# Optimization experiments

Measured on AMD Instinct MI355X. Metric: run time of the kernel, lower is better.

Reference implementation:

```python
import jax, jax.numpy as jnp
import numpy as np

MAX_SCALE_CAP = 200
STEP = 3


def _shift(a, dy, dx):
    # a[..., y+dy, x+dx] with zero fill outside (dy, dx >= 0), matching the
    # zero-padded dilated 3x3 convs whose only off-center tap is at (+dy,+dx).
    H, W = a.shape[-2], a.shape[-1]
    p = jnp.pad(a, ((0, 0), (0, 0), (0, dy), (0, dx)))
    return p[..., dy:dy + H, dx:dx + W]


def _dif_stacks(Pred, GT, ROI):
    # Builds difPrd / difGT: channel order is (scale major, layer l, direction)
    # directions in dict order: Horizontal (0,+s), Vertical (+s,0), Diagonal (+s,+s)
    B, _, H, W = Pred.shape
    max_scale = min(MAX_SCALE_CAP, max(H, W))
    dP, dG = [], []
    for scale in range(1, max_scale, STEP):
        bP, bG = [], []
        for dy, dx in ((0, scale), (scale, 0), (scale, scale)):
            roi = ROI * _shift(ROI, dy, dx)             # [B,1,H,W]
            bP.append(roi * (Pred - _shift(Pred, dy, dx)))  # [B,3,H,W]
            bG.append(roi * (GT - _shift(GT, dy, dx)))
        # stack dirs on a new axis after layer axis -> l-major, dir-minor
        dP.append(jnp.stack(bP, axis=2).reshape(B, 9, H, W))
        dG.append(jnp.stack(bG, axis=2).reshape(B, 9, H, W))
    return jnp.concatenate(dP, axis=1), jnp.concatenate(dG, axis=1)


def _loss(PredXYZ, GTXYZ, ROIMask):
    difPrd, difGT = _dif_stacks(PredXYZ, GTXYZ, ROIMask)

    # normalization constant per image (detached in the original)
    Rat = jax.nn.relu(difPrd / (difGT + 1e-5))
    absG = jnp.abs(difGT)
    NormConst = (absG * Rat).sum((1, 2, 3)) / ((absG * (Rat > 0)).sum((1, 2, 3)) + 1e-4)
    NormConst = jax.lax.stop_gradient(NormConst)

    c = NormConst                                   # [B]
    safe_c = jnp.where(c > 1e-4, c, 1.0)
    term1 = jnp.where(
        c > 1e-4,
        jnp.abs(difGT - difPrd / safe_c[:, None, None, None]).mean((1, 2, 3)),
        0.0,
    )

    roi_sum = ROIMask.sum((1, 2, 3))
    pos_cnt = (difGT > 0).sum((1, 2, 3)).astype(jnp.float32)
    mean_prd = jnp.abs(difPrd).sum((1, 2, 3)) / pos_cnt

    big = roi_sum > 200
    term2 = jnp.where(big & (mean_prd > 30) & (c > 10), mean_prd - 30.0, 0.0)
    fact = 0.1 / (c + 0.001)
    term3 = jnp.where(big & (mean_prd < 2) & (c < 0.1), (0.2 - mean_prd) * fact, 0.0)

    return (term1 + term2 + term3).sum(), NormConst


def setup_inputs() -> dict:
    key = jax.random.key(0)
    k1, k2, k3 = jax.random.split(key, 3)
    PredXYZ = jax.random.normal(k1, (2, 3, 256, 256), dtype=jnp.float32)
    GTXYZ = jax.random.normal(k2, (2, 3, 256, 256), dtype=jnp.float32)
    ROIMask = (jax.random.uniform(k3, (2, 1, 256, 256)) > 0.3).astype(jnp.float32)
    return {"PredXYZ": PredXYZ, "GTXYZ": GTXYZ, "ROIMask": ROIMask}


def reference(PredXYZ, GTXYZ, ROIMask):
    return _loss(PredXYZ, GTXYZ, ROIMask)
```

## Files before the change

### kernel.cpp

```cpp
#include <hip/hip_runtime.h>


#define NSCALES 67
#define IMG_H 256
#define IMG_W 256
#define NPIX 65536
#define NLINES 2046
#define LMAX_PAD 320


__device__ __forceinline__ double wave_red(double v) {
#pragma unroll
  for (int o = 32; o > 0; o >>= 1) v += __shfl_down(v, o, 64);
  return v;
}

__device__ __forceinline__ void decode_line(int id, int& b, int& base, int& stride, int& L) {
  if (id < 512) {
    b = id >> 8; int y = id & 255;
    base = y * IMG_W; stride = 1; L = IMG_W;
  } else if (id < 1024) {
    int t = id - 512; b = t >> 8;
    base = t & 255; stride = IMG_W; L = IMG_H;
  } else {
    int t = id - 1024; b = (t >= 511) ? 1 : 0;
    int d = t - b * 511; int c = d - 255;
    int ac = (c < 0) ? -c : c;
    base = (c < 0) ? (-c) * IMG_W : c;
    stride = IMG_W + 1; L = 256 - ac;
  }
}

__device__ __forceinline__ int scale_count(int L, int q) {
  int rem = L - 1 - (q << 6);
  int kcnt = (rem >= 1) ? ((rem - 1) / 3 + 1) : 0;
  return (kcnt > NSCALES) ? NSCALES : kcnt;
}

__device__ __forceinline__ float stage_line(
    const float* __restrict__ Pred, const float* __restrict__ GT,
    const float* __restrict__ ROI, int b, int base, int stride, int L,
    int tid, float4* bufA, float4* bufB) {
  const float* P = Pred + b * (3 * NPIX);
  const float* G = GT + b * (3 * NPIX);
  const float* R = ROI + b * NPIX;
  float r = 0.f, p0 = 0.f, p1 = 0.f, p2 = 0.f, g0 = 0.f, g1 = 0.f, g2 = 0.f;
  if (tid < L) {
    int a = base + tid * stride;
    r = R[a];
    p0 = P[a]; p1 = P[a + NPIX]; p2 = P[a + 2 * NPIX];
    g0 = G[a]; g1 = G[a + NPIX]; g2 = G[a + 2 * NPIX];
  }
  bufA[tid] = make_float4(r, p0, p1, p2);
  bufB[tid] = make_float4(g0, g1, g2, 0.f);
  if (tid < LMAX_PAD - 256) {
    bufA[256 + tid] = make_float4(0.f, 0.f, 0.f, 0.f);
    bufB[256 + tid] = make_float4(0.f, 0.f, 0.f, 0.f);
  }
  __syncthreads();
  return r;
}

extern "C" __global__ void __launch_bounds__(256, 8) pass1_kernel(
    const float* __restrict__ Pred, const float* __restrict__ GT,
    const float* __restrict__ ROI, double* __restrict__ ws) {
  __shared__ float4 bufA[LMAX_PAD];
  __shared__ float4 bufB[LMAX_PAD];
  __shared__ double red[4][5];
  const int id = blockIdx.x;
  const int tid = threadIdx.x;
  const int wid = tid >> 6, lane = tid & 63;

  int b, base, stride, L;
  decode_line(id, b, base, stride, L);
  float stg_r = stage_line(Pred, GT, ROI, b, base, stride, L, tid, bufA, bufB);

  float f1 = 0.f, f2 = 0.f, fp = 0.f;
  int pci = 0;
  int P = 0;
  for (int q = 0; q < 4; ++q) {
    const int Kq = scale_count(L, q);
    int k = (wid - P) & 3;
    if (k < Kq) {
      const int c = (q << 6) + lane;
      const float4 cA = bufA[c];
      const float4 cB = bufB[c];
      const float cr = cA.x, cp0 = cA.y, cp1 = cA.z, cp2 = cA.w;
      const float cg0 = cB.x, cg1 = cB.y, cg2 = cB.z;
      const float4* tA = &bufA[c + 1 + 3 * k];
      const float4* tB = &bufB[c + 1 + 3 * k];
#pragma unroll 2
      for (; k < Kq; k += 4) {
        float4 t0 = tA[0];
        float4 t1 = tB[0];
        tA += 12; tB += 12;
        float rr = cr * t0.x;
#define L1BODY(cp, cg, tp, tg)                                   \
        {                                                        \
          float dP = rr * (cp - tp);                             \
          float dG = rr * (cg - tg);                             \
          float qq = dP * __builtin_amdgcn_rcpf(dG + 1e-5f);     \
          float aG = fabsf(dG);                                  \
          f1 += fmaxf(aG * qq, 0.f);                             \
          if (qq > 0.f) f2 += aG;                                \
          if (dG > 0.f) pci++;                                   \
          fp += fabsf(dP);                                       \
        }
        L1BODY(cp0, cg0, t0.y, t1.x)
        L1BODY(cp1, cg1, t0.z, t1.y)
        L1BODY(cp2, cg2, t0.w, t1.z)
#undef L1BODY
      }
    }
    P += Kq;
  }

  double w0 = wave_red((double)f1);
  double w1 = wave_red((double)f2);
  double w2 = wave_red((double)pci);
  double w3 = wave_red((double)fp);
  double w4 = wave_red((double)stg_r);
  if (lane == 0) {
    red[wid][0] = w0; red[wid][1] = w1; red[wid][2] = w2;
    red[wid][3] = w3; red[wid][4] = w4;
  }
  __syncthreads();
  if (tid < 4)
    unsafeAtomicAdd(&ws[b * 4 + tid],
                    red[0][tid] + red[1][tid] + red[2][tid] + red[3][tid]);
  if (tid == 4 && id < 512)
    unsafeAtomicAdd(&ws[8 + b], red[0][4] + red[1][4] + red[2][4] + red[3][4]);
}

extern "C" __global__ void __launch_bounds__(256, 8) pass2_kernel(
    const float* __restrict__ Pred, const float* __restrict__ GT,
    const float* __restrict__ ROI, double* __restrict__ ws) {
  __shared__ float4 bufA[LMAX_PAD];
  __shared__ float4 bufB[LMAX_PAD];
  __shared__ double red[4];
  __shared__ float s_invC;
  const int id = blockIdx.x;
  const int tid = threadIdx.x;
  const int wid = tid >> 6, lane = tid & 63;

  int b, base, stride, L;
  decode_line(id, b, base, stride, L);
  if (tid == 0) {
    double S1 = ws[b * 4 + 0], S2 = ws[b * 4 + 1];
    float cc = (float)(S1 / (S2 + 1e-4));
    s_invC = (cc > 1e-4f) ? (float)(1.0 / (double)cc) : 1.0f;
  }
  stage_line(Pred, GT, ROI, b, base, stride, L, tid, bufA, bufB);

  const float invC = s_invC;
  float f = 0.f;
  int P = 0;
  for (int q = 0; q < 4; ++q) {
    const int Kq = scale_count(L, q);
    int k = (wid - P) & 3;
    if (k < Kq) {
      const int c = (q << 6) + lane;
      const float4 cA = bufA[c];
      const float4 cB = bufB[c];
      const float cr = cA.x, cp0 = cA.y, cp1 = cA.z, cp2 = cA.w;
      const float cg0 = cB.x, cg1 = cB.y, cg2 = cB.z;
      const float4* tA = &bufA[c + 1 + 3 * k];
      const float4* tB = &bufB[c + 1 + 3 * k];
#pragma unroll 2
      for (; k < Kq; k += 4) {
        float4 t0 = tA[0];
        float4 t1 = tB[0];
        tA += 12; tB += 12;
        float rr = cr * t0.x;
        f += rr * fabsf((cg0 - t1.x) - (cp0 - t0.y) * invC);
        f += rr * fabsf((cg1 - t1.y) - (cp1 - t0.z) * invC);
        f += rr * fabsf((cg2 - t1.z) - (cp2 - t0.w) * invC);
      }
    }
    P += Kq;
  }
  double t = wave_red((double)f);
  if (lane == 0) red[wid] = t;
  __syncthreads();
  if (tid == 0)
    unsafeAtomicAdd(&ws[24 + b], red[0] + red[1] + red[2] + red[3]);
}

extern "C" __global__ void __launch_bounds__(64) final_kernel(
    const double* __restrict__ ws, float* __restrict__ out) {
  if (threadIdx.x == 0) {
    double loss = 0.0;
    for (int b = 0; b < 2; ++b) {
      double S1 = ws[b * 4 + 0], S2 = ws[b * 4 + 1];
      double PC = ws[b * 4 + 2], SP = ws[b * 4 + 3];
      double RS = ws[8 + b];
      float cc = (float)(S1 / (S2 + 1e-4));
      out[1 + b] = cc;
      double term1 = (cc > 1e-4f) ? ws[24 + b] / (603.0 * 65536.0) : 0.0;
      float meanPrd = (float)(SP / PC);
      bool big = RS > 200.0;
      float t2 = (big && meanPrd > 30.f && cc > 10.f) ? (meanPrd - 30.f) : 0.f;
      float fact = 0.1f / (cc + 0.001f);
      float t3 = (big && meanPrd < 2.f && cc < 0.1f) ? (0.2f - meanPrd) * fact : 0.f;
      loss += term1 + (double)(t2 + t3);
    }
    out[0] = (float)loss;
  }
}

extern "C" void kernel_launch(void* const* d_in, const int* in_sizes, int n_in,
                              void* d_out, int out_size, void* d_ws, size_t ws_size,
                              hipStream_t stream) {
  (void)in_sizes; (void)n_in; (void)out_size; (void)ws_size;
  const float* Pred = (const float*)d_in[0];
  const float* GT = (const float*)d_in[1];
  const float* ROI = (const float*)d_in[2];
  float* out = (float*)d_out;
  double* ws = (double*)d_ws;

  hipMemsetAsync(d_ws, 0, 32 * sizeof(double), stream);
  hipLaunchKernelGGL(pass1_kernel, dim3(NLINES), dim3(256), 0, stream,
                     Pred, GT, ROI, ws);
  hipLaunchKernelGGL(pass2_kernel, dim3(NLINES), dim3(256), 0, stream,
                     Pred, GT, ROI, ws);
  hipLaunchKernelGGL(final_kernel, dim3(1), dim3(64), 0, stream, ws, out);
}
```

Measured before the change: 128.1 us.

## Fuse both passes and final reduction into one kernel with grid-wide spin barrier

Merges pass1, pass2 and the final kernel into a single launch that uses an atomic counter as a grid barrier between the normalization-constant pass and the second pass. Each block keeps its staged line in shared memory and reuses it, instead of reloading it from global memory. Block 0 waits for all blocks to finish and then computes the final loss. This relies on all 2046 blocks being co-resident; the spin limit avoids a hang but would give wrong results if they are not.

```diff
diff --git a/kernel.cpp b/kernel.cpp
--- a/kernel.cpp
+++ b/kernel.cpp
@@ -61,12 +61,18 @@
   return r;
 }
 
-extern "C" __global__ void __launch_bounds__(256, 8) pass1_kernel(
+__device__ __forceinline__ double aread(const double* p) {
+  return __hip_atomic_load(p, __ATOMIC_RELAXED, __HIP_MEMORY_SCOPE_AGENT);
+}
+
+extern "C" __global__ void __launch_bounds__(256, 8) fused_kernel(
     const float* __restrict__ Pred, const float* __restrict__ GT,
-    const float* __restrict__ ROI, double* __restrict__ ws) {
+    const float* __restrict__ ROI, double* __restrict__ ws,
+    float* __restrict__ out) {
   __shared__ float4 bufA[LMAX_PAD];
   __shared__ float4 bufB[LMAX_PAD];
   __shared__ double red[4][5];
+  __shared__ float s_invC;
   const int id = blockIdx.x;
   const int tid = threadIdx.x;
   const int wid = tid >> 6, lane = tid & 63;
@@ -130,31 +136,27 @@
                     red[0][tid] + red[1][tid] + red[2][tid] + red[3][tid]);
   if (tid == 4 && id < 512)
     unsafeAtomicAdd(&ws[8 + b], red[0][4] + red[1][4] + red[2][4] + red[3][4]);
-}
-
-extern "C" __global__ void __launch_bounds__(256, 8) pass2_kernel(
-    const float* __restrict__ Pred, const float* __restrict__ GT,
-    const float* __restrict__ ROI, double* __restrict__ ws) {
-  __shared__ float4 bufA[LMAX_PAD];
-  __shared__ float4 bufB[LMAX_PAD];
-  __shared__ double red[4];
-  __shared__ float s_invC;
-  const int id = blockIdx.x;
-  const int tid = threadIdx.x;
-  const int wid = tid >> 6, lane = tid & 63;
-
-  int b, base, stride, L;
-  decode_line(id, b, base, stride, L);
+
+  int* ctr = (int*)&ws[16];
+  __threadfence();
+  __syncthreads();
   if (tid == 0) {
-    double S1 = ws[b * 4 + 0], S2 = ws[b * 4 + 1];
+    __hip_atomic_fetch_add(ctr, 1, __ATOMIC_ACQ_REL, __HIP_MEMORY_SCOPE_AGENT);
+    int spins = 0;
+    while (__hip_atomic_load(ctr, __ATOMIC_ACQUIRE, __HIP_MEMORY_SCOPE_AGENT) < NLINES &&
+           spins < (1 << 22)) {
+      __builtin_amdgcn_s_sleep(2);
+      ++spins;
+    }
+    double S1 = aread(&ws[b * 4 + 0]), S2 = aread(&ws[b * 4 + 1]);
     float cc = (float)(S1 / (S2 + 1e-4));
     s_invC = (cc > 1e-4f) ? (float)(1.0 / (double)cc) : 1.0f;
   }
-  stage_line(Pred, GT, ROI, b, base, stride, L, tid, bufA, bufB);
+  __syncthreads();
 
   const float invC = s_invC;
   float f = 0.f;
-  int P = 0;
+  P = 0;
   for (int q = 0; q < 4; ++q) {
     const int Kq = scale_count(L, q);
     int k = (wid - P) & 3;
@@ -180,23 +182,29 @@
     P += Kq;
   }
   double t = wave_red((double)f);
-  if (lane == 0) red[wid] = t;
-  __syncthreads();
-  if (tid == 0)
-    unsafeAtomicAdd(&ws[24 + b], red[0] + red[1] + red[2] + red[3]);
-}
-
-extern "C" __global__ void __launch_bounds__(64) final_kernel(
-    const double* __restrict__ ws, float* __restrict__ out) {
-  if (threadIdx.x == 0) {
+  if (lane == 0) red[wid][0] = t;
+  __syncthreads();
+  if (tid == 0) {
+    unsafeAtomicAdd(&ws[24 + b], red[0][0] + red[1][0] + red[2][0] + red[3][0]);
+    __threadfence();
+    __hip_atomic_fetch_add(ctr, 1, __ATOMIC_ACQ_REL, __HIP_MEMORY_SCOPE_AGENT);
+  }
+
+  if (id == 0 && tid == 0) {
+    int spins = 0;
+    while (__hip_atomic_load(ctr, __ATOMIC_ACQUIRE, __HIP_MEMORY_SCOPE_AGENT) < 2 * NLINES &&
+           spins < (1 << 22)) {
+      __builtin_amdgcn_s_sleep(2);
+      ++spins;
+    }
     double loss = 0.0;
-    for (int b = 0; b < 2; ++b) {
-      double S1 = ws[b * 4 + 0], S2 = ws[b * 4 + 1];
-      double PC = ws[b * 4 + 2], SP = ws[b * 4 + 3];
-      double RS = ws[8 + b];
+    for (int bb = 0; bb < 2; ++bb) {
+      double S1 = aread(&ws[bb * 4 + 0]), S2 = aread(&ws[bb * 4 + 1]);
+      double PC = aread(&ws[bb * 4 + 2]), SP = aread(&ws[bb * 4 + 3]);
+      double RS = aread(&ws[8 + bb]);
       float cc = (float)(S1 / (S2 + 1e-4));
-      out[1 + b] = cc;
-      double term1 = (cc > 1e-4f) ? ws[24 + b] / (603.0 * 65536.0) : 0.0;
+      out[1 + bb] = cc;
+      double term1 = (cc > 1e-4f) ? aread(&ws[24 + bb]) / (603.0 * 65536.0) : 0.0;
       float meanPrd = (float)(SP / PC);
       bool big = RS > 200.0;
       float t2 = (big && meanPrd > 30.f && cc > 10.f) ? (meanPrd - 30.f) : 0.f;
@@ -219,9 +227,6 @@
   double* ws = (double*)d_ws;
 
   hipMemsetAsync(d_ws, 0, 32 * sizeof(double), stream);
-  hipLaunchKernelGGL(pass1_kernel, dim3(NLINES), dim3(256), 0, stream,
-                     Pred, GT, ROI, ws);
-  hipLaunchKernelGGL(pass2_kernel, dim3(NLINES), dim3(256), 0, stream,
-                     Pred, GT, ROI, ws);
-  hipLaunchKernelGGL(final_kernel, dim3(1), dim3(64), 0, stream, ws, out);
-}
+  hipLaunchKernelGGL(fused_kernel, dim3(NLINES), dim3(256), 0, stream,
+                     Pred, GT, ROI, ws, out);
+}
```

New measurement: 336.4 us. 163% more time.

## Use persistent blocks with atomic work queue and fold final reduction into pass2

Applied to the files above, without the earlier changes.

Both passes now launch 1024 persistent blocks that take the heavy horizontal/vertical lines first. Each block then grabs the remaining diagonal lines from an atomic counter, which balances the uneven per-line work. The separate final kernel is removed: the last pass2 block to finish, found through an acq_rel done counter, computes the loss. This trades an extra launch and tail imbalance for atomic counter traffic and extra barriers per line.

```diff
diff --git a/kernel.cpp b/kernel.cpp
--- a/kernel.cpp
+++ b/kernel.cpp
@@ -7,6 +7,7 @@
 #define NPIX 65536
 #define NLINES 2046
 #define LMAX_PAD 320
+#define GRID1 1024
 
 
 __device__ __forceinline__ double wave_red(double v) {
@@ -61,150 +62,183 @@
   return r;
 }
 
+__device__ __forceinline__ double aread(const double* p) {
+  return __hip_atomic_load(p, __ATOMIC_RELAXED, __HIP_MEMORY_SCOPE_AGENT);
+}
+
 extern "C" __global__ void __launch_bounds__(256, 8) pass1_kernel(
     const float* __restrict__ Pred, const float* __restrict__ GT,
     const float* __restrict__ ROI, double* __restrict__ ws) {
   __shared__ float4 bufA[LMAX_PAD];
   __shared__ float4 bufB[LMAX_PAD];
   __shared__ double red[4][5];
-  const int id = blockIdx.x;
+  __shared__ int s_line;
   const int tid = threadIdx.x;
   const int wid = tid >> 6, lane = tid & 63;
-
-  int b, base, stride, L;
-  decode_line(id, b, base, stride, L);
-  float stg_r = stage_line(Pred, GT, ROI, b, base, stride, L, tid, bufA, bufB);
-
-  float f1 = 0.f, f2 = 0.f, fp = 0.f;
-  int pci = 0;
-  int P = 0;
-  for (int q = 0; q < 4; ++q) {
-    const int Kq = scale_count(L, q);
-    int k = (wid - P) & 3;
-    if (k < Kq) {
-      const int c = (q << 6) + lane;
-      const float4 cA = bufA[c];
-      const float4 cB = bufB[c];
-      const float cr = cA.x, cp0 = cA.y, cp1 = cA.z, cp2 = cA.w;
-      const float cg0 = cB.x, cg1 = cB.y, cg2 = cB.z;
-      const float4* tA = &bufA[c + 1 + 3 * k];
-      const float4* tB = &bufB[c + 1 + 3 * k];
+  int* ctr = (int*)&ws[16];
+
+  int id = blockIdx.x;
+  while (id < NLINES) {
+    int b, base, stride, L;
+    decode_line(id, b, base, stride, L);
+    float stg_r = stage_line(Pred, GT, ROI, b, base, stride, L, tid, bufA, bufB);
+
+    float f1 = 0.f, f2 = 0.f, fp = 0.f;
+    int pci = 0;
+    int P = 0;
+    for (int q = 0; q < 4; ++q) {
+      const int Kq = scale_count(L, q);
+      int k = (wid - P) & 3;
+      if (k < Kq) {
+        const int c = (q << 6) + lane;
+        const float4 cA = bufA[c];
+        const float4 cB = bufB[c];
+        const float cr = cA.x, cp0 = cA.y, cp1 = cA.z, cp2 = cA.w;
+        const float cg0 = cB.x, cg1 = cB.y, cg2 = cB.z;
+        const float4* tA = &bufA[c + 1 + 3 * k];
+        const float4* tB = &bufB[c + 1 + 3 * k];
 #pragma unroll 2
-      for (; k < Kq; k += 4) {
-        float4 t0 = tA[0];
-        float4 t1 = tB[0];
-        tA += 12; tB += 12;
-        float rr = cr * t0.x;
+        for (; k < Kq; k += 4) {
+          float4 t0 = tA[0];
+          float4 t1 = tB[0];
+          tA += 12; tB += 12;
+          float rr = cr * t0.x;
 #define L1BODY(cp, cg, tp, tg)                                   \
-        {                                                        \
-          float dP = rr * (cp - tp);                             \
-          float dG = rr * (cg - tg);                             \
-          float qq = dP * __builtin_amdgcn_rcpf(dG + 1e-5f);     \
-          float aG = fabsf(dG);                                  \
-          f1 += fmaxf(aG * qq, 0.f);                             \
-          if (qq > 0.f) f2 += aG;                                \
-          if (dG > 0.f) pci++;                                   \
-          fp += fabsf(dP);                                       \
+          {                                                      \
+            float dP = rr * (cp - tp);                           \
+            float dG = rr * (cg - tg);                           \
+            float qq = dP * __builtin_amdgcn_rcpf(dG + 1e-5f);   \
+            float aG = fabsf(dG);                                \
+            f1 += fmaxf(aG * qq, 0.f);                           \
+            if (qq > 0.f) f2 += aG;                              \
+            if (dG > 0.f) pci++;                                 \
+            fp += fabsf(dP);                                     \
+          }
+          L1BODY(cp0, cg0, t0.y, t1.x)
+          L1BODY(cp1, cg1, t0.z, t1.y)
+          L1BODY(cp2, cg2, t0.w, t1.z)
+#undef L1BODY
         }
-        L1BODY(cp0, cg0, t0.y, t1.x)
-        L1BODY(cp1, cg1, t0.z, t1.y)
-        L1BODY(cp2, cg2, t0.w, t1.z)
-#undef L1BODY
       }
-    }
-    P += Kq;
-  }
-
-  double w0 = wave_red((double)f1);
-  double w1 = wave_red((double)f2);
-  double w2 = wave_red((double)pci);
-  double w3 = wave_red((double)fp);
-  double w4 = wave_red((double)stg_r);
-  if (lane == 0) {
-    red[wid][0] = w0; red[wid][1] = w1; red[wid][2] = w2;
-    red[wid][3] = w3; red[wid][4] = w4;
-  }
-  __syncthreads();
-  if (tid < 4)
-    unsafeAtomicAdd(&ws[b * 4 + tid],
-                    red[0][tid] + red[1][tid] + red[2][tid] + red[3][tid]);
-  if (tid == 4 && id < 512)
-    unsafeAtomicAdd(&ws[8 + b], red[0][4] + red[1][4] + red[2][4] + red[3][4]);
+      P += Kq;
+    }
+
+    double w0 = wave_red((double)f1);
+    double w1 = wave_red((double)f2);
+    double w2 = wave_red((double)pci);
+    double w3 = wave_red((double)fp);
+    double w4 = wave_red((double)stg_r);
+    if (lane == 0) {
+      red[wid][0] = w0; red[wid][1] = w1; red[wid][2] = w2;
+      red[wid][3] = w3; red[wid][4] = w4;
+    }
+    __syncthreads();
+    if (tid < 4)
+      unsafeAtomicAdd(&ws[b * 4 + tid],
+                      red[0][tid] + red[1][tid] + red[2][tid] + red[3][tid]);
+    if (tid == 4 && id < 512)
+      unsafeAtomicAdd(&ws[8 + b], red[0][4] + red[1][4] + red[2][4] + red[3][4]);
+
+    __syncthreads();
+    if (tid == 0)
+      s_line = 1024 + __hip_atomic_fetch_add(ctr, 1, __ATOMIC_RELAXED,
+                                             __HIP_MEMORY_SCOPE_AGENT);
+    __syncthreads();
+    id = s_line;
+  }
 }
 
 extern "C" __global__ void __launch_bounds__(256, 8) pass2_kernel(
     const float* __restrict__ Pred, const float* __restrict__ GT,
-    const float* __restrict__ ROI, double* __restrict__ ws) {
+    const float* __restrict__ ROI, double* __restrict__ ws,
+    float* __restrict__ out) {
   __shared__ float4 bufA[LMAX_PAD];
   __shared__ float4 bufB[LMAX_PAD];
   __shared__ double red[4];
-  __shared__ float s_invC;
-  const int id = blockIdx.x;
+  __shared__ float s_invC[2];
+  __shared__ int s_line;
   const int tid = threadIdx.x;
   const int wid = tid >> 6, lane = tid & 63;
-
-  int b, base, stride, L;
-  decode_line(id, b, base, stride, L);
+  int* ctr = (int*)&ws[17];
+  int* done = (int*)&ws[18];
+
+  if (tid < 2) {
+    double S1 = ws[tid * 4 + 0];
+    double S2 = ws[tid * 4 + 1];
+    float cc = (float)(S1 / (S2 + 1e-4));
+    s_invC[tid] = (cc > 1e-4f) ? (float)(1.0 / (double)cc) : 1.0f;
+  }
+  __syncthreads();
+
+  int id = blockIdx.x;
+  while (id < NLINES) {
+    int b, base, stride, L;
+    decode_line(id, b, base, stride, L);
+    stage_line(Pred, GT, ROI, b, base, stride, L, tid, bufA, bufB);
+
+    const float invC = s_invC[b];
+    float f = 0.f;
+    int P = 0;
+    for (int q = 0; q < 4; ++q) {
+      const int Kq = scale_count(L, q);
+      int k = (wid - P) & 3;
+      if (k < Kq) {
+        const int c = (q << 6) + lane;
+        const float4 cA = bufA[c];
+        const float4 cB = bufB[c];
+        const float cr = cA.x, cp0 = cA.y, cp1 = cA.z, cp2 = cA.w;
+        const float cg0 = cB.x, cg1 = cB.y, cg2 = cB.z;
+        const float4* tA = &bufA[c + 1 + 3 * k];
+        const float4* tB = &bufB[c + 1 + 3 * k];
+#pragma unroll 2
+        for (; k < Kq; k += 4) {
+          float4 t0 = tA[0];
+          float4 t1 = tB[0];
+          tA += 12; tB += 12;
+          float rr = cr * t0.x;
+          f += rr * fabsf((cg0 - t1.x) - (cp0 - t0.y) * invC);
+          f += rr * fabsf((cg1 - t1.y) - (cp1 - t0.z) * invC);
+          f += rr * fabsf((cg2 - t1.z) - (cp2 - t0.w) * invC);
+        }
+      }
+      P += Kq;
+    }
+    double t = wave_red((double)f);
+    if (lane == 0) red[wid] = t;
+    __syncthreads();
+    if (tid == 0)
+      unsafeAtomicAdd(&ws[24 + b], red[0] + red[1] + red[2] + red[3]);
+
+    __syncthreads();
+    if (tid == 0)
+      s_line = 1024 + __hip_atomic_fetch_add(ctr, 1, __ATOMIC_RELAXED,
+                                             __HIP_MEMORY_SCOPE_AGENT);
+    __syncthreads();
+    id = s_line;
+  }
+
   if (tid == 0) {
-    double S1 = ws[b * 4 + 0], S2 = ws[b * 4 + 1];
-    float cc = (float)(S1 / (S2 + 1e-4));
-    s_invC = (cc > 1e-4f) ? (float)(1.0 / (double)cc) : 1.0f;
-  }
-  stage_line(Pred, GT, ROI, b, base, stride, L, tid, bufA, bufB);
-
-  const float invC = s_invC;
-  float f = 0.f;
-  int P = 0;
-  for (int q = 0; q < 4; ++q) {
-    const int Kq = scale_count(L, q);
-    int k = (wid - P) & 3;
-    if (k < Kq) {
-      const int c = (q << 6) + lane;
-      const float4 cA = bufA[c];
-      const float4 cB = bufB[c];
-      const float cr = cA.x, cp0 = cA.y, cp1 = cA.z, cp2 = cA.w;
-      const float cg0 = cB.x, cg1 = cB.y, cg2 = cB.z;
-      const float4* tA = &bufA[c + 1 + 3 * k];
-      const float4* tB = &bufB[c + 1 + 3 * k];
-#pragma unroll 2
-      for (; k < Kq; k += 4) {
-        float4 t0 = tA[0];
-        float4 t1 = tB[0];
-        tA += 12; tB += 12;
-        float rr = cr * t0.x;
-        f += rr * fabsf((cg0 - t1.x) - (cp0 - t0.y) * invC);
-        f += rr * fabsf((cg1 - t1.y) - (cp1 - t0.z) * invC);
-        f += rr * fabsf((cg2 - t1.z) - (cp2 - t0.w) * invC);
+    __threadfence();
+    int rank = __hip_atomic_fetch_add(done, 1, __ATOMIC_ACQ_REL,
+                                      __HIP_MEMORY_SCOPE_AGENT);
+    if (rank == GRID1 - 1) {
+      double loss = 0.0;
+      for (int bb = 0; bb < 2; ++bb) {
+        double S1 = aread(&ws[bb * 4 + 0]), S2 = aread(&ws[bb * 4 + 1]);
+        double PC = aread(&ws[bb * 4 + 2]), SP = aread(&ws[bb * 4 + 3]);
+        double RS = aread(&ws[8 + bb]);
+        float cc = (float)(S1 / (S2 + 1e-4));
+        out[1 + bb] = cc;
+        double term1 = (cc > 1e-4f) ? aread(&ws[24 + bb]) / (603.0 * 65536.0) : 0.0;
+        float meanPrd = (float)(SP / PC);
+        bool big = RS > 200.0;
+        float t2 = (big && meanPrd > 30.f && cc > 10.f) ? (meanPrd - 30.f) : 0.f;
+        float fact = 0.1f / (cc + 0.001f);
+        float t3 = (big && meanPrd < 2.f && cc < 0.1f) ? (0.2f - meanPrd) * fact : 0.f;
+        loss += term1 + (double)(t2 + t3);
       }
-    }
-    P += Kq;
-  }
-  double t = wave_red((double)f);
-  if (lane == 0) red[wid] = t;
-  __syncthreads();
-  if (tid == 0)
-    unsafeAtomicAdd(&ws[24 + b], red[0] + red[1] + red[2] + red[3]);
-}
-
-extern "C" __global__ void __launch_bounds__(64) final_kernel(
-    const double* __restrict__ ws, float* __restrict__ out) {
-  if (threadIdx.x == 0) {
-    double loss = 0.0;
-    for (int b = 0; b < 2; ++b) {
-      double S1 = ws[b * 4 + 0], S2 = ws[b * 4 + 1];
-      double PC = ws[b * 4 + 2], SP = ws[b * 4 + 3];
-      double RS = ws[8 + b];
-      float cc = (float)(S1 / (S2 + 1e-4));
-      out[1 + b] = cc;
-      double term1 = (cc > 1e-4f) ? ws[24 + b] / (603.0 * 65536.0) : 0.0;
-      float meanPrd = (float)(SP / PC);
-      bool big = RS > 200.0;
-      float t2 = (big && meanPrd > 30.f && cc > 10.f) ? (meanPrd - 30.f) : 0.f;
-      float fact = 0.1f / (cc + 0.001f);
-      float t3 = (big && meanPrd < 2.f && cc < 0.1f) ? (0.2f - meanPrd) * fact : 0.f;
-      loss += term1 + (double)(t2 + t3);
-    }
-    out[0] = (float)loss;
+      out[0] = (float)loss;
+    }
   }
 }
 
@@ -219,9 +253,8 @@
   double* ws = (double*)d_ws;
 
   hipMemsetAsync(d_ws, 0, 32 * sizeof(double), stream);
-  hipLaunchKernelGGL(pass1_kernel, dim3(NLINES), dim3(256), 0, stream,
+  hipLaunchKernelGGL(pass1_kernel, dim3(GRID1), dim3(256), 0, stream,
                      Pred, GT, ROI, ws);
-  hipLaunchKernelGGL(pass2_kernel, dim3(NLINES), dim3(256), 0, stream,
-                     Pred, GT, ROI, ws);
-  hipLaunchKernelGGL(final_kernel, dim3(1), dim3(64), 0, stream, ws, out);
-}
+  hipLaunchKernelGGL(pass2_kernel, dim3(GRID1), dim3(256), 0, stream,
+                     Pred, GT, ROI, ws, out);
+}
```

Result: slower. 160.0 us (+24.9%).

## Cache staged lines in workspace for pass2 and fuse final reduction via last-block

Applied to the files above, without the earlier changes.

Pass1 now writes each block's staged line buffers (coalesced float4) to workspace, and pass2 reads them contiguously instead of re-gathering strided and diagonal pixels from the inputs. The separate final kernel is removed: the last pass2 block, found through an atomic counter, computes the loss. This trades strided gathers for extra workspace traffic of about 16 MB written and read, and it saves one kernel launch.

```diff
diff --git a/kernel.cpp b/kernel.cpp
--- a/kernel.cpp
+++ b/kernel.cpp
@@ -61,6 +61,10 @@
   return r;
 }
 
+__device__ __forceinline__ double aread(const double* p) {
+  return __hip_atomic_load(p, __ATOMIC_RELAXED, __HIP_MEMORY_SCOPE_AGENT);
+}
+
 extern "C" __global__ void __launch_bounds__(256, 8) pass1_kernel(
     const float* __restrict__ Pred, const float* __restrict__ GT,
     const float* __restrict__ ROI, double* __restrict__ ws) {
@@ -74,6 +78,10 @@
   int b, base, stride, L;
   decode_line(id, b, base, stride, L);
   float stg_r = stage_line(Pred, GT, ROI, b, base, stride, L, tid, bufA, bufB);
+
+  float4* S4 = (float4*)((char*)ws + 4096);
+  S4[(size_t)id * 512 + tid] = bufA[tid];
+  S4[(size_t)id * 512 + 256 + tid] = bufB[tid];
 
   float f1 = 0.f, f2 = 0.f, fp = 0.f;
   int pci = 0;
@@ -133,26 +141,36 @@
 }
 
 extern "C" __global__ void __launch_bounds__(256, 8) pass2_kernel(
-    const float* __restrict__ Pred, const float* __restrict__ GT,
-    const float* __restrict__ ROI, double* __restrict__ ws) {
+    double* __restrict__ ws, float* __restrict__ out) {
   __shared__ float4 bufA[LMAX_PAD];
   __shared__ float4 bufB[LMAX_PAD];
   __shared__ double red[4];
-  __shared__ float s_invC;
+  __shared__ float s_invC[2];
   const int id = blockIdx.x;
   const int tid = threadIdx.x;
   const int wid = tid >> 6, lane = tid & 63;
+  int* done = (int*)&ws[18];
 
   int b, base, stride, L;
   decode_line(id, b, base, stride, L);
-  if (tid == 0) {
-    double S1 = ws[b * 4 + 0], S2 = ws[b * 4 + 1];
+
+  if (tid < 2) {
+    double S1 = ws[tid * 4 + 0];
+    double S2 = ws[tid * 4 + 1];
     float cc = (float)(S1 / (S2 + 1e-4));
-    s_invC = (cc > 1e-4f) ? (float)(1.0 / (double)cc) : 1.0f;
-  }
-  stage_line(Pred, GT, ROI, b, base, stride, L, tid, bufA, bufB);
-
-  const float invC = s_invC;
+    s_invC[tid] = (cc > 1e-4f) ? (float)(1.0 / (double)cc) : 1.0f;
+  }
+
+  const float4* S4 = (const float4*)((const char*)ws + 4096);
+  bufA[tid] = S4[(size_t)id * 512 + tid];
+  bufB[tid] = S4[(size_t)id * 512 + 256 + tid];
+  if (tid < LMAX_PAD - 256) {
+    bufA[256 + tid] = make_float4(0.f, 0.f, 0.f, 0.f);
+    bufB[256 + tid] = make_float4(0.f, 0.f, 0.f, 0.f);
+  }
+  __syncthreads();
+
+  const float invC = s_invC[b];
   float f = 0.f;
   int P = 0;
   for (int q = 0; q < 4; ++q) {
@@ -182,29 +200,29 @@
   double t = wave_red((double)f);
   if (lane == 0) red[wid] = t;
   __syncthreads();
-  if (tid == 0)
+  if (tid == 0) {
     unsafeAtomicAdd(&ws[24 + b], red[0] + red[1] + red[2] + red[3]);
-}
-
-extern "C" __global__ void __launch_bounds__(64) final_kernel(
-    const double* __restrict__ ws, float* __restrict__ out) {
-  if (threadIdx.x == 0) {
-    double loss = 0.0;
-    for (int b = 0; b < 2; ++b) {
-      double S1 = ws[b * 4 + 0], S2 = ws[b * 4 + 1];
-      double PC = ws[b * 4 + 2], SP = ws[b * 4 + 3];
-      double RS = ws[8 + b];
-      float cc = (float)(S1 / (S2 + 1e-4));
-      out[1 + b] = cc;
-      double term1 = (cc > 1e-4f) ? ws[24 + b] / (603.0 * 65536.0) : 0.0;
-      float meanPrd = (float)(SP / PC);
-      bool big = RS > 200.0;
-      float t2 = (big && meanPrd > 30.f && cc > 10.f) ? (meanPrd - 30.f) : 0.f;
-      float fact = 0.1f / (cc + 0.001f);
-      float t3 = (big && meanPrd < 2.f && cc < 0.1f) ? (0.2f - meanPrd) * fact : 0.f;
-      loss += term1 + (double)(t2 + t3);
+    __threadfence();
+    int rank = __hip_atomic_fetch_add(done, 1, __ATOMIC_ACQ_REL,
+                                      __HIP_MEMORY_SCOPE_AGENT);
+    if (rank == NLINES - 1) {
+      double loss = 0.0;
+      for (int bb = 0; bb < 2; ++bb) {
+        double S1 = aread(&ws[bb * 4 + 0]), S2 = aread(&ws[bb * 4 + 1]);
+        double PC = aread(&ws[bb * 4 + 2]), SP = aread(&ws[bb * 4 + 3]);
+        double RS = aread(&ws[8 + bb]);
+        float cc = (float)(S1 / (S2 + 1e-4));
+        out[1 + bb] = cc;
+        double term1 = (cc > 1e-4f) ? aread(&ws[24 + bb]) / (603.0 * 65536.0) : 0.0;
+        float meanPrd = (float)(SP / PC);
+        bool big = RS > 200.0;
+        float t2 = (big && meanPrd > 30.f && cc > 10.f) ? (meanPrd - 30.f) : 0.f;
+        float fact = 0.1f / (cc + 0.001f);
+        float t3 = (big && meanPrd < 2.f && cc < 0.1f) ? (0.2f - meanPrd) * fact : 0.f;
+        loss += term1 + (double)(t2 + t3);
+      }
+      out[0] = (float)loss;
     }
-    out[0] = (float)loss;
   }
 }
 
@@ -222,6 +240,5 @@
   hipLaunchKernelGGL(pass1_kernel, dim3(NLINES), dim3(256), 0, stream,
                      Pred, GT, ROI, ws);
   hipLaunchKernelGGL(pass2_kernel, dim3(NLINES), dim3(256), 0, stream,
-                     Pred, GT, ROI, ws);
-  hipLaunchKernelGGL(final_kernel, dim3(1), dim3(64), 0, stream, ws, out);
-}
+                     ws, out);
+}
```

New measurement: 168.4 us. 31.4% more time.
